# Kernel optimization log

Hardware: AMD Instinct MI355X
Metric: run time of the kernel (lower is better)

The kernel has to match this reference:

```python
import jax, jax.numpy as jnp
import numpy as np
import math

B, S, D, H, W = 4, 8192, 1024, 16, 512  # batch, seq, d_model, heads, attention_window
HD = D // H


def setup_inputs() -> dict:
    key = jax.random.key(0)
    ks = jax.random.split(key, 5)
    scale = 0.02
    return {
        "x": jax.random.normal(ks[0], (B, S, D), dtype=jnp.float32),
        "wq": jax.random.normal(ks[1], (D, D), dtype=jnp.float32) * scale,
        "bq": jnp.zeros((D,), dtype=jnp.float32),
        "wk": jax.random.normal(ks[2], (D, D), dtype=jnp.float32) * scale,
        "bk": jnp.zeros((D,), dtype=jnp.float32),
        "wv": jax.random.normal(ks[3], (D, D), dtype=jnp.float32) * scale,
        "bv": jnp.zeros((D,), dtype=jnp.float32),
        "wo": jax.random.normal(ks[4], (D, D), dtype=jnp.float32) * scale,
        "bo": jnp.zeros((D,), dtype=jnp.float32),
    }


def reference(x, wq, bq, wk, bk, wv, bv, wo, bo):
    # torch Linear: y = x @ W.T + b
    q = (x @ wq.T + bq).reshape(B, S, H, HD)
    k = (x @ wk.T + bk).reshape(B, S, H, HD)
    v = (x @ wv.T + bv).reshape(B, S, H, HD)

    nb = S // W  # number of query blocks
    qb = q.reshape(B, nb, W, H, HD)

    # pad keys/values by W at the front so every block sees a 2W key window
    kp = jnp.pad(k, ((0, 0), (W, 0), (0, 0), (0, 0)))
    vp = jnp.pad(v, ((0, 0), (W, 0), (0, 0), (0, 0)))
    # padded key indices for block n: [n*W, n*W + 2W) <-> original [n*W - W, n*W + W)
    idx = jnp.arange(nb)[:, None] * W + jnp.arange(2 * W)[None, :]  # [nb, 2W]
    kb = kp[:, idx]  # [B, nb, 2W, H, HD]
    vb = vp[:, idx]  # [B, nb, 2W, H, HD]

    scores = jnp.einsum('bnqhd,bnkhd->bnhqk', qb, kb) / math.sqrt(HD)
    valid = (idx >= W)  # padded (out-of-range) keys only occur for block 0
    scores = jnp.where(valid[None, :, None, None, :], scores, -jnp.inf)
    attn = jax.nn.softmax(scores, axis=-1)  # softmax over the block's key window

    out = jnp.einsum('bnhqk,bnkhd->bnqhd', attn, vb).reshape(B, S, D)
    return out @ wo.T + bo
```

## Files before the change

kernel.cpp:

```cpp
#include <hip/hip_runtime.h>
#include <hip/hip_bf16.h>
#include <cstdint>

typedef __bf16 bf16;
typedef __attribute__((ext_vector_type(8))) __bf16 bf16x8;
typedef __attribute__((ext_vector_type(4))) __bf16 bf16x4;
typedef __attribute__((ext_vector_type(4))) float f32x4;
typedef __attribute__((ext_vector_type(16))) float f32x16;
typedef __attribute__((ext_vector_type(4))) unsigned int u32x4;

#define B_ 4
#define S_ 8192
#define D_ 1024
#define H_ 16
#define HD_ 64
#define W_ 512
#define M_ (B_*S_)

#define EXP2F(x) __builtin_amdgcn_exp2f(x)
#define MFMA16(a,b,c) __builtin_amdgcn_mfma_f32_16x16x32_bf16(a,b,c,0,0,0)
#define MFMA32(a,b,c) __builtin_amdgcn_mfma_f32_32x32x16_bf16(a,b,c,0,0,0)

__device__ __forceinline__ void async16(const void* g, void* l) {
  __builtin_amdgcn_global_load_lds(
      (const __attribute__((address_space(1))) unsigned int*)g,
      (__attribute__((address_space(3))) unsigned int*)l, 16, 0, 0);
}

__device__ __forceinline__ void cast_region(const float* __restrict__ in,
                                            bf16* __restrict__ out, int n4,
                                            int i0, int stride) {
  for (int i = i0; i < n4; i += stride) {
    f32x4 v = ((const f32x4*)in)[i];
    bf16x4 o = { (bf16)v[0], (bf16)v[1], (bf16)v[2], (bf16)v[3] };
    ((bf16x4*)out)[i] = o;
  }
}

__global__ void cast_all(const float* __restrict__ x,  bf16* __restrict__ xb,
                         const float* __restrict__ wq, bf16* __restrict__ wqb,
                         const float* __restrict__ wk, bf16* __restrict__ wkb,
                         const float* __restrict__ wv, bf16* __restrict__ wvb,
                         const float* __restrict__ wo, bf16* __restrict__ wob) {
  int i0 = blockIdx.x * blockDim.x + threadIdx.x;
  int stride = gridDim.x * blockDim.x;
  cast_region(x,  xb,  M_*D_/4, i0, stride);
  cast_region(wq, wqb, D_*D_/4, i0, stride);
  cast_region(wk, wkb, D_*D_/4, i0, stride);
  cast_region(wv, wvb, D_*D_/4, i0, stride);
  cast_region(wo, wob, D_*D_/4, i0, stride);
}

template<int MODE>
__global__ void __launch_bounds__(512, 2) gemm_bt(
    const bf16* __restrict__ A, const bf16* __restrict__ Bw,
    const float* __restrict__ bias, void* __restrict__ outp, float scale)
{
  constexpr int K = D_, N = D_;
  __shared__ char lds[4 * 32768];
  int bid = blockIdx.x;
  int nid = (bid & 7) * 64 + (bid >> 3);
  int bm = nid >> 2, bn = nid & 3;
  const int tid = threadIdx.x, lane = tid & 63;
  const int w = tid >> 6, wr = w >> 2, wc = w & 3;
  f32x4 acc[8][4] = {};
  const char* Ab = (const char*)(A + (size_t)bm * 256 * K);
  const char* Bb = (const char*)(Bw + (size_t)bn * 256 * K);
  const int srow16 = tid & 15;
  const int skb    = ((tid >> 4) & 3) * 16;

  auto stageA = [&](int t2) {
#pragma unroll
    for (int j = 0; j < 2; ++j) {
      int f = j * 8 + (tid >> 6);
      char* dst = lds + (t2 & 3) * 32768 + j * 8192 + tid * 16;
      async16(Ab + (size_t)(f * 16 + srow16) * (K * 2) + t2 * 64 + skb, dst);
    }
  };
  auto stageB = [&](int t2) {
#pragma unroll
    for (int j = 0; j < 2; ++j) {
      int f = j * 8 + (tid >> 6);
      char* dst = lds + (t2 & 3) * 32768 + 16384 + j * 8192 + tid * 16;
      async16(Bb + (size_t)(f * 16 + srow16) * (K * 2) + t2 * 64 + skb, dst);
    }
  };

  auto compute = [&](int sl, int qm) {
    const char* ab = lds + sl * 32768;
    const char* bb = ab + 16384;
    bf16x8 a[4], b[4];
#pragma unroll
    for (int r = 0; r < 4; ++r)
      a[r] = *(const bf16x8*)(ab + (wr * 8 + qm * 4 + r) * 1024 + lane * 16);
#pragma unroll
    for (int c = 0; c < 4; ++c)
      b[c] = *(const bf16x8*)(bb + (wc * 4 + c) * 1024 + lane * 16);
    asm volatile("s_waitcnt lgkmcnt(0)" ::: "memory");
    __builtin_amdgcn_sched_barrier(0);
    __builtin_amdgcn_s_setprio(1);
#pragma unroll
    for (int r = 0; r < 4; ++r)
#pragma unroll
      for (int c = 0; c < 4; ++c)
        acc[qm * 4 + r][c] = MFMA16(a[r], b[c], acc[qm * 4 + r][c]);
    __builtin_amdgcn_s_setprio(0);
  };

  stageA(0); stageB(0); stageA(1); stageB(1);

#pragma unroll 1
  for (int it = 0; it < 16; ++it) {
    int e = 2 * it;
    bool full = (it < 15);
    if (full) { stageA(e + 2);
      asm volatile("s_waitcnt vmcnt(6)" ::: "memory");
    } else {
      asm volatile("s_waitcnt vmcnt(4)" ::: "memory");
    }
    __builtin_amdgcn_s_barrier();
    compute(e & 3, 0);
    __builtin_amdgcn_s_barrier();
    if (full) stageB(e + 2);
    __builtin_amdgcn_s_barrier();
    compute(e & 3, 1);
    __builtin_amdgcn_s_barrier();
    if (full) { stageA(e + 3);
      asm volatile("s_waitcnt vmcnt(6)" ::: "memory");
    } else {
      asm volatile("s_waitcnt vmcnt(0)" ::: "memory");
    }
    __builtin_amdgcn_s_barrier();
    compute((e + 1) & 3, 0);
    __builtin_amdgcn_s_barrier();
    if (full) stageB(e + 3);
    __builtin_amdgcn_s_barrier();
    compute((e + 1) & 3, 1);
    __builtin_amdgcn_s_barrier();
  }

  int row0 = bm * 256 + wr * 128, col0 = bn * 256 + wc * 64;
  int rsub = (lane >> 4) * 4;
#pragma unroll
  for (int cb = 0; cb < 4; ++cb) {
    int col = col0 + cb * 16 + (lane & 15);
    float bz = bias[col];
#pragma unroll
    for (int rb = 0; rb < 8; ++rb) {
#pragma unroll
      for (int reg = 0; reg < 4; ++reg) {
        int row = row0 + rb * 16 + rsub + reg;
        float v = (acc[rb][cb][reg] + bz) * scale;
        if (MODE == 0) {
          ((bf16*)outp)[(size_t)row * N + col] = (bf16)v;
        } else if (MODE == 1) {
          ((bf16*)outp)[((size_t)(row >> 13) * D_ + col) * S_ + (row & (S_-1))] = (bf16)v;
        } else {
          ((float*)outp)[(size_t)row * N + col] = v;
        }
      }
    }
  }
}

__global__ void __launch_bounds__(256, 4) attn_kernel(
    const bf16* __restrict__ Q, const bf16* __restrict__ Kb,
    const bf16* __restrict__ Vt, bf16* __restrict__ Ao)
{
  __shared__ char Klds[2][8192];
  __shared__ char Vlds[2][8192];
  int x = blockIdx.x;
  int qt = (x >> 3) & 3;
  int g  = (x & 7) + 8 * (x >> 5);
  int h = g & 15, n = (g >> 4) & 15, b = g >> 8;
  int tid = threadIdx.x, lane = tid & 63, w = tid >> 6;
  int hi = lane >> 5, qv = lane & 31;
  int qrow = n * W_ + qt * 128 + w * 32;

  const bf16* Qrow = Q + ((size_t)(b * S_ + qrow + qv)) * D_ + h * 64;
  bf16x8 Qf[4];
#pragma unroll
  for (int s = 0; s < 4; ++s) Qf[s] = *(const bf16x8*)(Qrow + s * 16 + hi * 8);

  const bf16* Kg = Kb + ((size_t)b * S_) * D_ + h * 64;
  const bf16* Vg = Vt + ((size_t)(b * H_ + h) * HD_) * S_;

  const int srow = tid >> 3;
  const int sseg = (tid & 7) ^ (srow & 7);
  const int fswq = (qv & 7) << 4;

  f32x16 O0 = {}, O1 = {};
  float l_r = 0.f;

  const int c0 = (n == 0) ? 8 : 0;
  const int ksbase = (n - 1) * W_;

  auto stage = [&](int c) {
    int ks = ksbase + c * 64;
    int so = (c & 1) * 8192;
    const bf16* kr = Kg + (size_t)(ks + srow) * D_ + sseg * 8;
    async16(kr,                    &Klds[0][0] + so + tid * 16);
    async16(kr + 32 * D_,          &Klds[0][0] + so + 4096 + tid * 16);
    const bf16* vr = Vg + (size_t)srow * S_ + ks + sseg * 8;
    async16(vr,                    &Vlds[0][0] + so + tid * 16);
    async16(vr + (size_t)32 * S_,  &Vlds[0][0] + so + 4096 + tid * 16);
  };

  stage(c0);
  asm volatile("s_waitcnt vmcnt(0)" ::: "memory");
  __builtin_amdgcn_s_barrier();

#pragma unroll 1
  for (int c = c0; c < 16; ++c) {
    if (c + 1 < 16) stage(c + 1);
    const char* kbuf = &Klds[0][0] + (c & 1) * 8192;
    const char* vbuf = &Vlds[0][0] + (c & 1) * 8192;
    f32x16 C0 = {}, C1 = {};
    __builtin_amdgcn_s_setprio(1);
#pragma unroll
    for (int s = 0; s < 4; ++s) {
      bf16x8 k0 = *(const bf16x8*)(kbuf + qv * 128        + ((s * 32 + hi * 16) ^ fswq));
      bf16x8 k1 = *(const bf16x8*)(kbuf + (32 + qv) * 128 + ((s * 32 + hi * 16) ^ fswq));
      C0 = MFMA32(k0, Qf[s], C0);
      C1 = MFMA32(k1, Qf[s], C1);
    }
    __builtin_amdgcn_s_setprio(0);
    float p0[16], p1[16];
#pragma unroll
    for (int r = 0; r < 16; ++r) {
      p0[r] = EXP2F(C0[r]);
      p1[r] = EXP2F(C1[r]);
    }
    float q0[8];
#pragma unroll
    for (int i = 0; i < 8; ++i)
      q0[i] = (p0[2*i] + p0[2*i+1]) + (p1[2*i] + p1[2*i+1]);
    l_r += ((q0[0] + q0[1]) + (q0[2] + q0[3])) + ((q0[4] + q0[5]) + (q0[6] + q0[7]));
    unsigned int L0[8], L1[8];
#pragma unroll
    for (int t = 0; t < 8; ++t) {
      asm("v_cvt_pk_bf16_f32 %0, %1, %2" : "=v"(L0[t]) : "v"(p0[2*t]), "v"(p0[2*t+1]));
      asm("v_cvt_pk_bf16_f32 %0, %1, %2" : "=v"(L1[t]) : "v"(p1[2*t]), "v"(p1[2*t+1]));
    }
    asm volatile("v_permlane32_swap_b32 %0, %1" : "+v"(L0[0]), "+v"(L0[2]));
    asm volatile("v_permlane32_swap_b32 %0, %1" : "+v"(L0[1]), "+v"(L0[3]));
    asm volatile("v_permlane32_swap_b32 %0, %1" : "+v"(L0[4]), "+v"(L0[6]));
    asm volatile("v_permlane32_swap_b32 %0, %1" : "+v"(L0[5]), "+v"(L0[7]));
    asm volatile("v_permlane32_swap_b32 %0, %1" : "+v"(L1[0]), "+v"(L1[2]));
    asm volatile("v_permlane32_swap_b32 %0, %1" : "+v"(L1[1]), "+v"(L1[3]));
    asm volatile("v_permlane32_swap_b32 %0, %1" : "+v"(L1[4]), "+v"(L1[6]));
    asm volatile("v_permlane32_swap_b32 %0, %1" : "+v"(L1[5]), "+v"(L1[7]));
    u32x4 F[2][2];
    F[0][0] = u32x4{L0[0], L0[1], L0[2], L0[3]};
    F[0][1] = u32x4{L0[4], L0[5], L0[6], L0[7]};
    F[1][0] = u32x4{L1[0], L1[1], L1[2], L1[3]};
    F[1][1] = u32x4{L1[4], L1[5], L1[6], L1[7]};
    __builtin_amdgcn_s_setprio(1);
#pragma unroll
    for (int T = 0; T < 2; ++T)
#pragma unroll
      for (int s = 0; s < 2; ++s) {
        bf16x8 pf = *(bf16x8*)&F[T][s];
        int kbyteoff = T * 64 + s * 32 + hi * 16;
        bf16x8 v0 = *(const bf16x8*)(vbuf + qv * 128        + (kbyteoff ^ fswq));
        bf16x8 v1 = *(const bf16x8*)(vbuf + (32 + qv) * 128 + (kbyteoff ^ fswq));
        O0 = MFMA32(v0, pf, O0);
        O1 = MFMA32(v1, pf, O1);
      }
    __builtin_amdgcn_s_setprio(0);
    asm volatile("s_waitcnt vmcnt(0)" ::: "memory");
    __builtin_amdgcn_s_barrier();
  }
  float lt = l_r + __shfl_xor(l_r, 32);
  float inv = 1.0f / lt;
  size_t obase = ((size_t)(b * S_ + qrow + qv)) * D_ + h * 64;
#pragma unroll
  for (int ot = 0; ot < 2; ++ot) {
#pragma unroll
    for (int rq = 0; rq < 4; ++rq) {
      int hd = ot * 32 + 8 * rq + 4 * hi;
      bf16x4 ov;
#pragma unroll
      for (int j = 0; j < 4; ++j) {
        float val = (ot == 0 ? O0[rq*4 + j] : O1[rq*4 + j]) * inv;
        ov[j] = (bf16)val;
      }
      *(bf16x4*)(Ao + obase + hd) = ov;
    }
  }
}

extern "C" void kernel_launch(void* const* d_in, const int* in_sizes, int n_in,
                              void* d_out, int out_size, void* d_ws, size_t ws_size,
                              hipStream_t stream) {
  const float* x  = (const float*)d_in[0];
  const float* wq = (const float*)d_in[1];
  const float* bq = (const float*)d_in[2];
  const float* wk = (const float*)d_in[3];
  const float* bk = (const float*)d_in[4];
  const float* wv = (const float*)d_in[5];
  const float* bv = (const float*)d_in[6];
  const float* wo = (const float*)d_in[7];
  const float* bo = (const float*)d_in[8];
  float* out = (float*)d_out;

  char* ws = (char*)d_ws;
  const size_t sz = (size_t)M_ * D_ * 2;
  bf16* xb  = (bf16*)(ws + 0*sz);
  bf16* qb  = (bf16*)(ws + 1*sz);
  bf16* kb  = (bf16*)(ws + 2*sz);
  bf16* vt  = (bf16*)(ws + 3*sz);
  bf16* ao  = (bf16*)(ws + 4*sz);
  bf16* wqb = (bf16*)(ws + 5*sz);
  bf16* wkb = wqb + (size_t)D_*D_;
  bf16* wvb = wkb + (size_t)D_*D_;
  bf16* wob = wvb + (size_t)D_*D_;

  cast_all<<<2048, 256, 0, stream>>>(x, xb, wq, wqb, wk, wkb, wv, wvb, wo, wob);

  gemm_bt<0><<<512, 512, 0, stream>>>(xb, wqb, bq, qb, 0.125f * 1.44269504f);
  gemm_bt<0><<<512, 512, 0, stream>>>(xb, wkb, bk, kb, 1.0f);
  gemm_bt<1><<<512, 512, 0, stream>>>(xb, wvb, bv, vt, 1.0f);

  attn_kernel<<<4096, 256, 0, stream>>>(qb, kb, vt, ao);

  gemm_bt<2><<<512, 512, 0, stream>>>(ao, wob, bo, out, 1.0f);
}
```

Measured before the change: 540.6 us.

## Restructure GEMM mainloop to K=64 double-buffered stages with quadrant ping-pong

Each GEMM pipeline stage now covers 64 K-elements instead of 32, with two 64KB LDS buffers in place of four 32KB ones. Every iteration is split into four MFMA quadrants that reuse A and B fragments held in registers. Each quadrant's LDS reads are interleaved with async global loads of the next stage, one quarter of the tile at a time. The aim is fewer barriers and waitcnt points per K step and more reuse of loaded fragments. The cost is higher register pressure and a shallower prefetch distance (one stage ahead rather than two).

```diff
diff --git a/kernel.cpp b/kernel.cpp
--- a/kernel.cpp
+++ b/kernel.cpp
@@ -56,8 +56,8 @@
     const bf16* __restrict__ A, const bf16* __restrict__ Bw,
     const float* __restrict__ bias, void* __restrict__ outp, float scale)
 {
-  constexpr int K = D_, N = D_;
-  __shared__ char lds[4 * 32768];
+  constexpr int K = D_;
+  __shared__ char lds[2 * 65536];
   int bid = blockIdx.x;
   int nid = (bid & 7) * 64 + (bid >> 3);
   int bm = nid >> 2, bn = nid & 3;
@@ -66,91 +66,131 @@
   f32x4 acc[8][4] = {};
   const char* Ab = (const char*)(A + (size_t)bm * 256 * K);
   const char* Bb = (const char*)(Bw + (size_t)bn * 256 * K);
-  const int srow16 = tid & 15;
-  const int skb    = ((tid >> 4) & 3) * 16;
-
-  auto stageA = [&](int t2) {
+  const int fr = tid & 15;
+  const int fk = ((tid >> 4) & 3) * 16;
+  const int fj = tid >> 6;
+
+  auto stageHalf = [&](int t2, int which) {
+    const char* src = (which < 2) ? Ab : Bb;
+    int h = which & 1;
+    char* dst = lds + (t2 & 1) * 65536 + which * 16384;
 #pragma unroll
     for (int j = 0; j < 2; ++j) {
-      int f = j * 8 + (tid >> 6);
-      char* dst = lds + (t2 & 3) * 32768 + j * 8192 + tid * 16;
-      async16(Ab + (size_t)(f * 16 + srow16) * (K * 2) + t2 * 64 + skb, dst);
+      int f = j * 8 + fj;
+      async16(src + (size_t)(h * 128 + (f >> 1) * 16 + fr) * (K * 2)
+                  + (size_t)t2 * 128 + (f & 1) * 64 + fk,
+              dst + f * 1024 + (tid & 63) * 16);
     }
   };
-  auto stageB = [&](int t2) {
-#pragma unroll
-    for (int j = 0; j < 2; ++j) {
-      int f = j * 8 + (tid >> 6);
-      char* dst = lds + (t2 & 3) * 32768 + 16384 + j * 8192 + tid * 16;
-      async16(Bb + (size_t)(f * 16 + srow16) * (K * 2) + t2 * 64 + skb, dst);
-    }
-  };
-
-  auto compute = [&](int sl, int qm) {
-    const char* ab = lds + sl * 32768;
-    const char* bb = ab + 16384;
-    bf16x8 a[4], b[4];
-#pragma unroll
-    for (int r = 0; r < 4; ++r)
-      a[r] = *(const bf16x8*)(ab + (wr * 8 + qm * 4 + r) * 1024 + lane * 16);
-#pragma unroll
-    for (int c = 0; c < 4; ++c)
-      b[c] = *(const bf16x8*)(bb + (wc * 4 + c) * 1024 + lane * 16);
+
+  stageHalf(0, 0); stageHalf(0, 1); stageHalf(0, 2); stageHalf(0, 3);
+
+  bf16x8 a[8], b0[4], b1[4];
+#pragma unroll 1
+  for (int t = 0; t < 16; ++t) {
+    const char* sl = lds + (t & 1) * 65536;
+    const char* sa = sl + wr * 16384;
+    const char* sb = sl + 32768 + (wc >> 1) * 16384;
+    const int cb = (wc & 1) * 4;
+    bool full = (t < 15);
+    if (full) stageHalf(t + 1, 0);
+    if (full) asm volatile("s_waitcnt vmcnt(2)" ::: "memory");
+    else      asm volatile("s_waitcnt vmcnt(0)" ::: "memory");
+    __builtin_amdgcn_s_barrier();
+#pragma unroll
+    for (int r = 0; r < 4; ++r) {
+      a[2*r]   = *(const bf16x8*)(sa + (r*2+0)*1024 + lane*16);
+      a[2*r+1] = *(const bf16x8*)(sa + (r*2+1)*1024 + lane*16);
+    }
+#pragma unroll
+    for (int c = 0; c < 2; ++c) {
+      b0[2*c]   = *(const bf16x8*)(sb + ((cb+c)*2+0)*1024 + lane*16);
+      b0[2*c+1] = *(const bf16x8*)(sb + ((cb+c)*2+1)*1024 + lane*16);
+    }
     asm volatile("s_waitcnt lgkmcnt(0)" ::: "memory");
     __builtin_amdgcn_sched_barrier(0);
     __builtin_amdgcn_s_setprio(1);
 #pragma unroll
     for (int r = 0; r < 4; ++r)
 #pragma unroll
-      for (int c = 0; c < 4; ++c)
-        acc[qm * 4 + r][c] = MFMA16(a[r], b[c], acc[qm * 4 + r][c]);
-    __builtin_amdgcn_s_setprio(0);
-  };
-
-  stageA(0); stageB(0); stageA(1); stageB(1);
-
-#pragma unroll 1
-  for (int it = 0; it < 16; ++it) {
-    int e = 2 * it;
-    bool full = (it < 15);
-    if (full) { stageA(e + 2);
-      asm volatile("s_waitcnt vmcnt(6)" ::: "memory");
-    } else {
-      asm volatile("s_waitcnt vmcnt(4)" ::: "memory");
-    }
-    __builtin_amdgcn_s_barrier();
-    compute(e & 3, 0);
-    __builtin_amdgcn_s_barrier();
-    if (full) stageB(e + 2);
-    __builtin_amdgcn_s_barrier();
-    compute(e & 3, 1);
-    __builtin_amdgcn_s_barrier();
-    if (full) { stageA(e + 3);
-      asm volatile("s_waitcnt vmcnt(6)" ::: "memory");
-    } else {
-      asm volatile("s_waitcnt vmcnt(0)" ::: "memory");
-    }
-    __builtin_amdgcn_s_barrier();
-    compute((e + 1) & 3, 0);
-    __builtin_amdgcn_s_barrier();
-    if (full) stageB(e + 3);
-    __builtin_amdgcn_s_barrier();
-    compute((e + 1) & 3, 1);
-    __builtin_amdgcn_s_barrier();
-  }
-
+      for (int c = 0; c < 2; ++c) {
+        acc[r][c] = MFMA16(a[2*r],   b0[2*c],   acc[r][c]);
+        acc[r][c] = MFMA16(a[2*r+1], b0[2*c+1], acc[r][c]);
+      }
+    __builtin_amdgcn_s_setprio(0);
+    __builtin_amdgcn_s_barrier();
+#pragma unroll
+    for (int r = 0; r < 4; ++r) {
+      a[2*r]   = *(const bf16x8*)(sa + ((4+r)*2+0)*1024 + lane*16);
+      a[2*r+1] = *(const bf16x8*)(sa + ((4+r)*2+1)*1024 + lane*16);
+    }
+    if (full) stageHalf(t + 1, 1);
+    __builtin_amdgcn_s_barrier();
+    asm volatile("s_waitcnt lgkmcnt(0)" ::: "memory");
+    __builtin_amdgcn_sched_barrier(0);
+    __builtin_amdgcn_s_setprio(1);
+#pragma unroll
+    for (int r = 0; r < 4; ++r)
+#pragma unroll
+      for (int c = 0; c < 2; ++c) {
+        acc[4+r][c] = MFMA16(a[2*r],   b0[2*c],   acc[4+r][c]);
+        acc[4+r][c] = MFMA16(a[2*r+1], b0[2*c+1], acc[4+r][c]);
+      }
+    __builtin_amdgcn_s_setprio(0);
+    __builtin_amdgcn_s_barrier();
+#pragma unroll
+    for (int c = 0; c < 2; ++c) {
+      b1[2*c]   = *(const bf16x8*)(sb + ((cb+2+c)*2+0)*1024 + lane*16);
+      b1[2*c+1] = *(const bf16x8*)(sb + ((cb+2+c)*2+1)*1024 + lane*16);
+    }
+    if (full) stageHalf(t + 1, 2);
+    __builtin_amdgcn_s_barrier();
+    asm volatile("s_waitcnt lgkmcnt(0)" ::: "memory");
+    __builtin_amdgcn_sched_barrier(0);
+    __builtin_amdgcn_s_setprio(1);
+#pragma unroll
+    for (int r = 0; r < 4; ++r)
+#pragma unroll
+      for (int c = 0; c < 2; ++c) {
+        acc[4+r][2+c] = MFMA16(a[2*r],   b1[2*c],   acc[4+r][2+c]);
+        acc[4+r][2+c] = MFMA16(a[2*r+1], b1[2*c+1], acc[4+r][2+c]);
+      }
+    __builtin_amdgcn_s_setprio(0);
+    __builtin_amdgcn_s_barrier();
+#pragma unroll
+    for (int r = 0; r < 4; ++r) {
+      a[2*r]   = *(const bf16x8*)(sa + (r*2+0)*1024 + lane*16);
+      a[2*r+1] = *(const bf16x8*)(sa + (r*2+1)*1024 + lane*16);
+    }
+    if (full) stageHalf(t + 1, 3);
+    __builtin_amdgcn_s_barrier();
+    asm volatile("s_waitcnt lgkmcnt(0)" ::: "memory");
+    __builtin_amdgcn_sched_barrier(0);
+    __builtin_amdgcn_s_setprio(1);
+#pragma unroll
+    for (int r = 0; r < 4; ++r)
+#pragma unroll
+      for (int c = 0; c < 2; ++c) {
+        acc[r][2+c] = MFMA16(a[2*r],   b1[2*c],   acc[r][2+c]);
+        acc[r][2+c] = MFMA16(a[2*r+1], b1[2*c+1], acc[r][2+c]);
+      }
+    __builtin_amdgcn_s_setprio(0);
+    __builtin_amdgcn_s_barrier();
+  }
+
+  constexpr int N = D_;
   int row0 = bm * 256 + wr * 128, col0 = bn * 256 + wc * 64;
   int rsub = (lane >> 4) * 4;
 #pragma unroll
-  for (int cb = 0; cb < 4; ++cb) {
-    int col = col0 + cb * 16 + (lane & 15);
+  for (int cf = 0; cf < 4; ++cf) {
+    int col = col0 + cf * 16 + (lane & 15);
     float bz = bias[col];
 #pragma unroll
-    for (int rb = 0; rb < 8; ++rb) {
+    for (int rf = 0; rf < 8; ++rf) {
 #pragma unroll
       for (int reg = 0; reg < 4; ++reg) {
-        int row = row0 + rb * 16 + rsub + reg;
-        float v = (acc[rb][cb][reg] + bz) * scale;
+        int row = row0 + rf * 16 + rsub + reg;
+        float v = (acc[rf][cf][reg] + bz) * scale;
         if (MODE == 0) {
           ((bf16*)outp)[(size_t)row * N + col] = (bf16)v;
         } else if (MODE == 1) {
```

Result: slower. 570.9 us (+5.6%).
